# Kernel optimization log

Measured on AMD Instinct MI355X. Metric: run time of the kernel, lower is better.

The kernel has to match this reference:

```python
import jax, jax.numpy as jnp
import numpy as np

N, C, L, D, F = 8, 128, 512, 64, 512
ATTN_W = 64
LN_EPS = 1e-5
ATTN_EPS = 1e-6


def _xavier(k, shape):
    lim = float(np.sqrt(6.0 / (shape[0] + shape[1])))
    return jax.random.uniform(k, shape, jnp.float32, -lim, lim)


def setup_inputs() -> dict:
    key = jax.random.key(0)
    ks = jax.random.split(key, 8)
    return dict(
        x=jax.random.normal(ks[0], (N, C, L), jnp.float32),
        Wx=_xavier(ks[1], (C, D)),
        Wt=_xavier(ks[2], (C, D)),
        bh=jnp.zeros((D,), jnp.float32),
        Wa=_xavier(ks[3], (D, 1)),
        ba=jnp.zeros((1,), jnp.float32),
        W0=_xavier(ks[4], (C, F)),
        b0=jnp.zeros((F,), jnp.float32),
        W1=_xavier(ks[5], (F, C)),
        b1=jnp.zeros((C,), jnp.float32),
        g0=jnp.ones((C,), jnp.float32),
        be0=jnp.zeros((C,), jnp.float32),
        g1=jnp.ones((C,), jnp.float32),
        be1=jnp.zeros((C,), jnp.float32),
    )


def _layernorm(y, g, b):
    mu = jnp.mean(y, axis=-1, keepdims=True)
    var = jnp.var(y, axis=-1, keepdims=True)
    return (y - mu) * jax.lax.rsqrt(var + LN_EPS) * g + b


def reference(x, Wx, Wt, bh, Wa, ba, W0, b0, W1, b1, g0, be0, g1, be1):
    xt = jnp.transpose(x, (0, 2, 1))  # (N, L, C)
    q = jnp.einsum('nlc,cd->nld', xt, Wt)  # (N, L, D)
    k = jnp.einsum('nlc,cd->nld', xt, Wx)  # (N, L, D)
    # additive (Bahdanau) scores: h is the large (N, L, L, D) intermediate
    h = jnp.tanh(q[:, :, None, :] + k[:, None, :, :] + bh)
    e = jnp.einsum('nlmd,d->nlm', h, Wa[:, 0]) + ba[0]  # (N, L, L)
    e = jnp.exp(e - jnp.max(e, axis=-1, keepdims=True))
    # local band mask: tril(w//2 - 1) & triu(-w//2) on (row i, col j)
    dij = jnp.arange(L)[None, :] - jnp.arange(L)[:, None]  # j - i
    mask = (dij <= ATTN_W // 2 - 1) & (dij >= -(ATTN_W // 2))
    e = jnp.where(mask, e, 0.0)
    a = e / (jnp.sum(e, axis=-1, keepdims=True) + ATTN_EPS)  # (N, L, L)
    v = jnp.einsum('nlm,nmc->nlc', a, xt)  # (N, L, C)
    x2 = _layernorm(v + xt, g0, be0)
    x3 = jnp.einsum('nlf,fc->nlc', jax.nn.relu(jnp.einsum('nlc,cf->nlf', x2, W0) + b0), W1) + b1
    x4 = _layernorm(x3 + x2, g1, be1)
    return (jnp.transpose(x4, (0, 2, 1)), a)
```

## Files before the change

### kernel.cpp

```cpp
#include <hip/hip_runtime.h>
#include <cstddef>


__global__ __launch_bounds__(256) void prep_kernel(
    const float* __restrict__ x, const float* __restrict__ Wt,
    const float* __restrict__ Wx, float* __restrict__ xt,
    float* __restrict__ q, float* __restrict__ k) {
  __shared__ float xs[128][17];
  int tid = threadIdx.x;
  int bz = blockIdx.x;
  int n = bz >> 6;
  int t6 = bz & 63;
  int l0 = (t6 >> 1) << 4;
  int which = t6 & 1;

  for (int idx = tid; idx < 512; idx += 256) {
    int c = idx >> 2, v = idx & 3;
    float4 d4 = *(const float4*)(x + ((size_t)n * 128 + c) * 512 + l0 + 4 * v);
    xs[c][4 * v + 0] = d4.x; xs[c][4 * v + 1] = d4.y;
    xs[c][4 * v + 2] = d4.z; xs[c][4 * v + 3] = d4.w;
  }
  __syncthreads();

  if (which == 0) {
    for (int idx = tid; idx < 2048; idx += 256) {
      int c = idx & 127, jj = idx >> 7;
      xt[((size_t)n * 512 + l0 + jj) * 128 + c] = xs[c][jj];
    }
  }

  const float* W = which ? Wx : Wt;
  float* dst = which ? k : q;
  int r = tid >> 4;
  int f0 = (tid & 15) << 2;
  float acc[4] = {0.f, 0.f, 0.f, 0.f};
#pragma unroll 4
  for (int cc = 0; cc < 128; cc++) {
    float xv = xs[cc][r];
    float4 w = *(const float4*)(W + cc * 64 + f0);
    acc[0] += xv * w.x; acc[1] += xv * w.y;
    acc[2] += xv * w.z; acc[3] += xv * w.w;
  }
  *(float4*)(dst + ((size_t)n * 512 + l0 + r) * 64 + f0) =
      make_float4(acc[0], acc[1], acc[2], acc[3]);
}

__global__ __launch_bounds__(512, 4) void attn_ffn_fused_kernel(
    const float* __restrict__ q, const float* __restrict__ k,
    const float* __restrict__ bh, const float* __restrict__ Wa,
    const float* __restrict__ ba, const float* __restrict__ xt,
    const float* __restrict__ g0, const float* __restrict__ be0,
    const float* __restrict__ W0, const float* __restrict__ b0,
    const float* __restrict__ W1, const float* __restrict__ b1,
    const float* __restrict__ g1, const float* __restrict__ be1,
    float* __restrict__ a, float* __restrict__ out) {
  __shared__ __align__(16) char smem[61440];
  __shared__ __align__(16) float xstT[128][12];
  __shared__ __align__(16) float avT[71][10];
  __shared__ __align__(16) float was[64];

  float (*ks)[68] = (float(*)[68])smem;
  float (*qs)[64] = (float(*)[64])(smem + 19328);
  float (*tstT)[12] = (float(*)[12])smem;
  float (*part)[8][128] = (float(*)[8][128])(smem + 24576);
  float (*ys)[128] = (float(*)[128])(smem + 57344);

  int tid = threadIdx.x;
  int w = tid >> 6, lane = tid & 63;
  size_t rbase = (size_t)blockIdx.x * 8;
  int n = (int)(rbase >> 9);
  int i0 = (int)(rbase & 511);
  int jlo0 = i0 - 32;

  if (tid < 64) was[tid] = Wa[tid];
  for (int idx = tid; idx < 71 * 10; idx += 512) ((float*)avT)[idx] = 0.f;
  if (tid < 128) {
    int r = tid >> 4, d4 = (tid & 15) << 2;
    float4 qv = *(const float4*)(q + ((size_t)n * 512 + i0 + r) * 64 + d4);
    float4 bv = *(const float4*)(bh + d4);
    *(float4*)(&qs[r][d4]) =
        make_float4(qv.x + bv.x, qv.y + bv.y, qv.z + bv.z, qv.w + bv.w);
  }
  for (int idx = tid; idx < 71 * 16; idx += 512) {
    int row = idx >> 4, d4 = (idx & 15) << 2;
    int j = jlo0 + row;
    float4 v = make_float4(0.f, 0.f, 0.f, 0.f);
    if (j >= 0 && j < 512)
      v = *(const float4*)(k + ((size_t)n * 512 + j) * 64 + d4);
    *(float4*)(&ks[row][d4]) = v;
  }
  __syncthreads();

  {
    int r = w;
    int i = i0 + r;
    int j = jlo0 + r + lane;
    bool valid = (j >= 0 && j < 512);
    const float* krow = &ks[r + lane][0];
    float e = 0.f;
#pragma unroll
    for (int d4 = 0; d4 < 64; d4 += 4) {
      float4 kv = *(const float4*)(krow + d4);
      float4 qv = *(const float4*)(&qs[r][d4]);
      float4 wv = *(const float4*)(&was[d4]);
      float h0 = qv.x + kv.x, h1 = qv.y + kv.y;
      float h2 = qv.z + kv.z, h3 = qv.w + kv.w;
      float t0 = 1.f - 2.f * __builtin_amdgcn_rcpf(__expf(2.f * h0) + 1.f);
      float t1 = 1.f - 2.f * __builtin_amdgcn_rcpf(__expf(2.f * h1) + 1.f);
      float t2 = 1.f - 2.f * __builtin_amdgcn_rcpf(__expf(2.f * h2) + 1.f);
      float t3 = 1.f - 2.f * __builtin_amdgcn_rcpf(__expf(2.f * h3) + 1.f);
      e += wv.x * t0 + wv.y * t1 + wv.z * t2 + wv.w * t3;
    }
    e += ba[0];
    if (!valid) e = -1e30f;

    float m = e;
    for (int o = 32; o > 0; o >>= 1) m = fmaxf(m, __shfl_xor(m, o, 64));
    float ex = valid ? __expf(e - m) : 0.f;
    float s = ex;
    for (int o = 32; o > 0; o >>= 1) s += __shfl_xor(s, o, 64);
    float aw = ex / (s + 1e-6f);
    avT[r + lane][r] = aw;

    float* arow = a + ((size_t)n * 512 + i) * 512;
    int jlo = i - 32;
#pragma unroll
    for (int t = 0; t < 2; t++) {
      int col0 = 4 * lane + 256 * t;
      float4 v;
      { int jr = col0 + 0 - jlo; int jc = min(max(jr, 0), 63); v.x = (jr >= 0 && jr < 64) ? avT[r + jc][r] : 0.f; }
      { int jr = col0 + 1 - jlo; int jc = min(max(jr, 0), 63); v.y = (jr >= 0 && jr < 64) ? avT[r + jc][r] : 0.f; }
      { int jr = col0 + 2 - jlo; int jc = min(max(jr, 0), 63); v.z = (jr >= 0 && jr < 64) ? avT[r + jc][r] : 0.f; }
      { int jr = col0 + 3 - jlo; int jc = min(max(jr, 0), 63); v.w = (jr >= 0 && jr < 64) ? avT[r + jc][r] : 0.f; }
      *(float4*)(arow + col0) = v;
    }
  }
  __syncthreads();

  {
    int c = tid & 127;
    int rh = tid >> 7;
    int r0 = 2 * rh;
    const float* xtn = xt + (size_t)n * 512 * 128;
    float acc0 = 0.f, acc1 = 0.f;
    for (int col = r0; col <= r0 + 64; col++) {
      int jj = jlo0 + col;
      int jc = min(max(jj, 0), 511);
      float xv = xtn[(size_t)jc * 128 + c];
      float2 av2 = *(const float2*)(&avT[col][r0]);
      acc0 += av2.x * xv;
      acc1 += av2.y * xv;
    }
    float res0 = xtn[(size_t)(i0 + r0) * 128 + c];
    float res1 = xtn[(size_t)(i0 + r0 + 1) * 128 + c];
    *(float2*)(&xstT[c][r0]) = make_float2(acc0 + res0, acc1 + res1);
  }
  __syncthreads();

  {
    float a0 = xstT[lane][w], a1 = xstT[lane + 64][w];
    float s = a0 + a1, s2 = a0 * a0 + a1 * a1;
    for (int o = 32; o > 0; o >>= 1) {
      s += __shfl_xor(s, o, 64);
      s2 += __shfl_xor(s2, o, 64);
    }
    float mu = s * (1.f / 128.f);
    float var = s2 * (1.f / 128.f) - mu * mu;
    float rs = rsqrtf(var + 1e-5f);
    xstT[lane][w] = (a0 - mu) * rs * g0[lane] + be0[lane];
    xstT[lane + 64][w] = (a1 - mu) * rs * g0[lane + 64] + be0[lane + 64];
  }
  __syncthreads();

  {
    int g = lane & 15;
    int kq = lane >> 4;
    int f0 = (16 * w + g) << 2;
    float acc[8][4];
#pragma unroll
    for (int i = 0; i < 8; i++)
#pragma unroll
      for (int u = 0; u < 4; u++) acc[i][u] = 0.f;
    int ccb = kq << 5;
#pragma unroll 4
    for (int cc = ccb; cc < ccb + 32; cc++) {
      float4 xa = *(const float4*)(&xstT[cc][0]);
      float4 xb = *(const float4*)(&xstT[cc][4]);
      float4 wv = *(const float4*)(W0 + (size_t)cc * 512 + f0);
      acc[0][0] += xa.x * wv.x; acc[0][1] += xa.x * wv.y; acc[0][2] += xa.x * wv.z; acc[0][3] += xa.x * wv.w;
      acc[1][0] += xa.y * wv.x; acc[1][1] += xa.y * wv.y; acc[1][2] += xa.y * wv.z; acc[1][3] += xa.y * wv.w;
      acc[2][0] += xa.z * wv.x; acc[2][1] += xa.z * wv.y; acc[2][2] += xa.z * wv.z; acc[2][3] += xa.z * wv.w;
      acc[3][0] += xa.w * wv.x; acc[3][1] += xa.w * wv.y; acc[3][2] += xa.w * wv.z; acc[3][3] += xa.w * wv.w;
      acc[4][0] += xb.x * wv.x; acc[4][1] += xb.x * wv.y; acc[4][2] += xb.x * wv.z; acc[4][3] += xb.x * wv.w;
      acc[5][0] += xb.y * wv.x; acc[5][1] += xb.y * wv.y; acc[5][2] += xb.y * wv.z; acc[5][3] += xb.y * wv.w;
      acc[6][0] += xb.z * wv.x; acc[6][1] += xb.z * wv.y; acc[6][2] += xb.z * wv.z; acc[6][3] += xb.z * wv.w;
      acc[7][0] += xb.w * wv.x; acc[7][1] += xb.w * wv.y; acc[7][2] += xb.w * wv.z; acc[7][3] += xb.w * wv.w;
    }
#pragma unroll
    for (int i = 0; i < 8; i++)
#pragma unroll
      for (int u = 0; u < 4; u++) {
        float v = acc[i][u];
        v += __shfl_xor(v, 16, 64);
        v += __shfl_xor(v, 32, 64);
        acc[i][u] = v;
      }
    int f = f0 + kq;
    float bb = b0[f];
    float r0v[8];
#pragma unroll
    for (int i = 0; i < 8; i++) {
      float v = (kq == 0) ? acc[i][0] : (kq == 1) ? acc[i][1]
              : (kq == 2) ? acc[i][2] : acc[i][3];
      r0v[i] = fmaxf(v + bb, 0.f);
    }
    *(float4*)(&tstT[f][0]) = make_float4(r0v[0], r0v[1], r0v[2], r0v[3]);
    *(float4*)(&tstT[f][4]) = make_float4(r0v[4], r0v[5], r0v[6], r0v[7]);
  }
  __syncthreads();

  {
    int c0 = (lane & 31) << 2;
    int rh = lane >> 5;
    float acc[4][4];
#pragma unroll
    for (int i = 0; i < 4; i++)
#pragma unroll
      for (int u = 0; u < 4; u++) acc[i][u] = 0.f;
    const float* W1p = W1 + (size_t)w * 64 * 128;
    int tb = w << 6;
#pragma unroll 4
    for (int t = 0; t < 64; t++) {
      float4 tv = *(const float4*)(&tstT[tb + t][4 * rh]);
      float4 wv = *(const float4*)(W1p + (size_t)t * 128 + c0);
      acc[0][0] += tv.x * wv.x; acc[0][1] += tv.x * wv.y; acc[0][2] += tv.x * wv.z; acc[0][3] += tv.x * wv.w;
      acc[1][0] += tv.y * wv.x; acc[1][1] += tv.y * wv.y; acc[1][2] += tv.y * wv.z; acc[1][3] += tv.y * wv.w;
      acc[2][0] += tv.z * wv.x; acc[2][1] += tv.z * wv.y; acc[2][2] += tv.z * wv.z; acc[2][3] += tv.z * wv.w;
      acc[3][0] += tv.w * wv.x; acc[3][1] += tv.w * wv.y; acc[3][2] += tv.w * wv.z; acc[3][3] += tv.w * wv.w;
    }
#pragma unroll
    for (int i = 0; i < 4; i++) {
      *(float4*)(&part[w][4 * rh + i][c0]) =
          make_float4(acc[i][0], acc[i][1], acc[i][2], acc[i][3]);
    }
  }
  __syncthreads();

  if (tid < 256) {
    int r = tid >> 5, c0 = (tid & 31) << 2;
    float4 s = make_float4(0.f, 0.f, 0.f, 0.f);
#pragma unroll
    for (int ko = 0; ko < 8; ko++) {
      float4 p = *(const float4*)(&part[ko][r][c0]);
      s.x += p.x; s.y += p.y; s.z += p.z; s.w += p.w;
    }
    float4 bv = *(const float4*)(b1 + c0);
    s.x += bv.x + xstT[c0 + 0][r];
    s.y += bv.y + xstT[c0 + 1][r];
    s.z += bv.z + xstT[c0 + 2][r];
    s.w += bv.w + xstT[c0 + 3][r];
    *(float4*)(&ys[r][c0]) = s;
  }
  __syncthreads();

  {
    float a0 = ys[w][lane], a1 = ys[w][lane + 64];
    float s = a0 + a1, s2 = a0 * a0 + a1 * a1;
    for (int o = 32; o > 0; o >>= 1) {
      s += __shfl_xor(s, o, 64);
      s2 += __shfl_xor(s2, o, 64);
    }
    float mu = s * (1.f / 128.f);
    float var = s2 * (1.f / 128.f) - mu * mu;
    float rs = rsqrtf(var + 1e-5f);
    ys[w][lane] = (a0 - mu) * rs * g1[lane] + be1[lane];
    ys[w][lane + 64] = (a1 - mu) * rs * g1[lane + 64] + be1[lane + 64];
  }
  __syncthreads();

  {
    int c = tid >> 2, tq = tid & 3;
    *(float2*)(out + ((size_t)n * 128 + c) * 512 + i0 + 2 * tq) =
        make_float2(ys[2 * tq][c], ys[2 * tq + 1][c]);
  }
}

extern "C" void kernel_launch(void* const* d_in, const int* in_sizes, int n_in,
                              void* d_out, int out_size, void* d_ws, size_t ws_size,
                              hipStream_t stream) {
  const float* x   = (const float*)d_in[0];
  const float* Wx  = (const float*)d_in[1];
  const float* Wt  = (const float*)d_in[2];
  const float* bh  = (const float*)d_in[3];
  const float* Wa  = (const float*)d_in[4];
  const float* ba  = (const float*)d_in[5];
  const float* W0  = (const float*)d_in[6];
  const float* b0  = (const float*)d_in[7];
  const float* W1  = (const float*)d_in[8];
  const float* b1  = (const float*)d_in[9];
  const float* g0  = (const float*)d_in[10];
  const float* be0 = (const float*)d_in[11];
  const float* g1  = (const float*)d_in[12];
  const float* be1 = (const float*)d_in[13];

  float* outx = (float*)d_out;
  float* outa = outx + (size_t)524288;

  float* ws = (float*)d_ws;
  float* xt = ws;
  float* q  = xt + 524288;
  float* k  = q + 262144;

  prep_kernel<<<512, 256, 0, stream>>>(x, Wt, Wx, xt, q, k);
  attn_ffn_fused_kernel<<<512, 512, 0, stream>>>(
      q, k, bh, Wa, ba, xt, g0, be0, W0, b0, W1, b1, g1, be1, outa, outx);
}
```

Baseline: 124.9 us.

## Drop xt workspace, stage x window in shared memory and prefetch FFN weights

The prep kernel no longer writes a transposed copy of x to global memory. Instead each attention block loads its 72-row window of x directly into a padded shared tile and uses it for the banded weighted sum and the residual. The prep kernel now computes q and k together in one 512-thread block. The W0/W1 loops gain register double-buffered weight prefetch, and the bias plus residual reduction is fused into the second layernorm, which removes one barrier. The cost is more shared memory packed into overlapping smem regions, and strided uncoalesced global reads when filling the x tile.

Result: no change. 124.7 us (-0.1%).

```diff
diff --git a/kernel.cpp b/kernel.cpp
--- a/kernel.cpp
+++ b/kernel.cpp
@@ -2,37 +2,29 @@
 #include <cstddef>
 
 
-__global__ __launch_bounds__(256) void prep_kernel(
+__global__ __launch_bounds__(512) void prep_kernel(
     const float* __restrict__ x, const float* __restrict__ Wt,
-    const float* __restrict__ Wx, float* __restrict__ xt,
-    float* __restrict__ q, float* __restrict__ k) {
+    const float* __restrict__ Wx, float* __restrict__ q,
+    float* __restrict__ k) {
   __shared__ float xs[128][17];
   int tid = threadIdx.x;
-  int bz = blockIdx.x;
-  int n = bz >> 6;
-  int t6 = bz & 63;
-  int l0 = (t6 >> 1) << 4;
-  int which = t6 & 1;
-
-  for (int idx = tid; idx < 512; idx += 256) {
-    int c = idx >> 2, v = idx & 3;
+  int n = blockIdx.x >> 5;
+  int l0 = (blockIdx.x & 31) << 4;
+
+  {
+    int c = tid >> 2, v = tid & 3;
     float4 d4 = *(const float4*)(x + ((size_t)n * 128 + c) * 512 + l0 + 4 * v);
     xs[c][4 * v + 0] = d4.x; xs[c][4 * v + 1] = d4.y;
     xs[c][4 * v + 2] = d4.z; xs[c][4 * v + 3] = d4.w;
   }
   __syncthreads();
 
-  if (which == 0) {
-    for (int idx = tid; idx < 2048; idx += 256) {
-      int c = idx & 127, jj = idx >> 7;
-      xt[((size_t)n * 512 + l0 + jj) * 128 + c] = xs[c][jj];
-    }
-  }
-
-  const float* W = which ? Wx : Wt;
-  float* dst = which ? k : q;
-  int r = tid >> 4;
-  int f0 = (tid & 15) << 2;
+  int half = tid >> 8;
+  int t = tid & 255;
+  int r = t >> 4;
+  int f0 = (t & 15) << 2;
+  const float* W = half ? Wx : Wt;
+  float* dst = half ? k : q;
   float acc[4] = {0.f, 0.f, 0.f, 0.f};
 #pragma unroll 4
   for (int cc = 0; cc < 128; cc++) {
@@ -46,9 +38,9 @@
 }
 
 __global__ __launch_bounds__(512, 4) void attn_ffn_fused_kernel(
-    const float* __restrict__ q, const float* __restrict__ k,
-    const float* __restrict__ bh, const float* __restrict__ Wa,
-    const float* __restrict__ ba, const float* __restrict__ xt,
+    const float* __restrict__ x, const float* __restrict__ q,
+    const float* __restrict__ k, const float* __restrict__ bh,
+    const float* __restrict__ Wa, const float* __restrict__ ba,
     const float* __restrict__ g0, const float* __restrict__ be0,
     const float* __restrict__ W0, const float* __restrict__ b0,
     const float* __restrict__ W1, const float* __restrict__ b1,
@@ -60,7 +52,8 @@
   __shared__ __align__(16) float was[64];
 
   float (*ks)[68] = (float(*)[68])smem;
-  float (*qs)[64] = (float(*)[64])(smem + 19328);
+  float (*qs)[64] = (float(*)[64])(smem + 19312);
+  float (*xtw)[132] = (float(*)[132])(smem + 21360);
   float (*tstT)[12] = (float(*)[12])smem;
   float (*part)[8][128] = (float(*)[8][128])(smem + 24576);
   float (*ys)[128] = (float(*)[128])(smem + 57344);
@@ -88,6 +81,24 @@
     if (j >= 0 && j < 512)
       v = *(const float4*)(k + ((size_t)n * 512 + j) * 64 + d4);
     *(float4*)(&ks[row][d4]) = v;
+  }
+  for (int t = tid; t < 128 * 18; t += 512) {
+    int c = t / 18;
+    int u = t - c * 18;
+    int row = 4 * u;
+    int j0 = jlo0 + row;
+    const float* xp = x + ((size_t)n * 128 + c) * 512;
+    float4 v = make_float4(0.f, 0.f, 0.f, 0.f);
+    if (j0 >= 0 && j0 + 3 < 512) {
+      v = *(const float4*)(xp + j0);
+    } else {
+      if (j0 + 0 >= 0 && j0 + 0 < 512) v.x = xp[j0 + 0];
+      if (j0 + 1 >= 0 && j0 + 1 < 512) v.y = xp[j0 + 1];
+      if (j0 + 2 >= 0 && j0 + 2 < 512) v.z = xp[j0 + 2];
+      if (j0 + 3 >= 0 && j0 + 3 < 512) v.w = xp[j0 + 3];
+    }
+    xtw[row + 0][c] = v.x; xtw[row + 1][c] = v.y;
+    xtw[row + 2][c] = v.z; xtw[row + 3][c] = v.w;
   }
   __syncthreads();
 
@@ -119,8 +130,7 @@
     float ex = valid ? __expf(e - m) : 0.f;
     float s = ex;
     for (int o = 32; o > 0; o >>= 1) s += __shfl_xor(s, o, 64);
-    float aw = ex / (s + 1e-6f);
-    avT[r + lane][r] = aw;
+    avT[r + lane][r] = ex / (s + 1e-6f);
 
     float* arow = a + ((size_t)n * 512 + i) * 512;
     int jlo = i - 32;
@@ -139,20 +149,18 @@
 
   {
     int c = tid & 127;
-    int rh = tid >> 7;
-    int r0 = 2 * rh;
-    const float* xtn = xt + (size_t)n * 512 * 128;
+    int r0 = (tid >> 7) << 1;
     float acc0 = 0.f, acc1 = 0.f;
-    for (int col = r0; col <= r0 + 64; col++) {
-      int jj = jlo0 + col;
-      int jc = min(max(jj, 0), 511);
-      float xv = xtn[(size_t)jc * 128 + c];
+#pragma unroll 5
+    for (int m = 0; m < 65; m++) {
+      int col = r0 + m;
+      float xv = xtw[col][c];
       float2 av2 = *(const float2*)(&avT[col][r0]);
       acc0 += av2.x * xv;
       acc1 += av2.y * xv;
     }
-    float res0 = xtn[(size_t)(i0 + r0) * 128 + c];
-    float res1 = xtn[(size_t)(i0 + r0 + 1) * 128 + c];
+    float res0 = xtw[32 + r0][c];
+    float res1 = xtw[33 + r0][c];
     *(float2*)(&xstT[c][r0]) = make_float2(acc0 + res0, acc1 + res1);
   }
   __syncthreads();
@@ -176,25 +184,41 @@
     int g = lane & 15;
     int kq = lane >> 4;
     int f0 = (16 * w + g) << 2;
+    int ccb = kq << 5;
+    const float* w0p = W0 + (size_t)ccb * 512 + f0;
     float acc[8][4];
 #pragma unroll
     for (int i = 0; i < 8; i++)
 #pragma unroll
       for (int u = 0; u < 4; u++) acc[i][u] = 0.f;
-    int ccb = kq << 5;
-#pragma unroll 4
-    for (int cc = ccb; cc < ccb + 32; cc++) {
-      float4 xa = *(const float4*)(&xstT[cc][0]);
-      float4 xb = *(const float4*)(&xstT[cc][4]);
-      float4 wv = *(const float4*)(W0 + (size_t)cc * 512 + f0);
-      acc[0][0] += xa.x * wv.x; acc[0][1] += xa.x * wv.y; acc[0][2] += xa.x * wv.z; acc[0][3] += xa.x * wv.w;
-      acc[1][0] += xa.y * wv.x; acc[1][1] += xa.y * wv.y; acc[1][2] += xa.y * wv.z; acc[1][3] += xa.y * wv.w;
-      acc[2][0] += xa.z * wv.x; acc[2][1] += xa.z * wv.y; acc[2][2] += xa.z * wv.z; acc[2][3] += xa.z * wv.w;
-      acc[3][0] += xa.w * wv.x; acc[3][1] += xa.w * wv.y; acc[3][2] += xa.w * wv.z; acc[3][3] += xa.w * wv.w;
-      acc[4][0] += xb.x * wv.x; acc[4][1] += xb.x * wv.y; acc[4][2] += xb.x * wv.z; acc[4][3] += xb.x * wv.w;
-      acc[5][0] += xb.y * wv.x; acc[5][1] += xb.y * wv.y; acc[5][2] += xb.y * wv.z; acc[5][3] += xb.y * wv.w;
-      acc[6][0] += xb.z * wv.x; acc[6][1] += xb.z * wv.y; acc[6][2] += xb.z * wv.z; acc[6][3] += xb.z * wv.w;
-      acc[7][0] += xb.w * wv.x; acc[7][1] += xb.w * wv.y; acc[7][2] += xb.w * wv.z; acc[7][3] += xb.w * wv.w;
+
+    float4 wbuf[4];
+#pragma unroll
+    for (int p = 0; p < 4; p++)
+      wbuf[p] = *(const float4*)(w0p + (size_t)p * 512);
+#pragma unroll
+    for (int c4 = 0; c4 < 8; c4++) {
+      float4 cur0 = wbuf[0], cur1 = wbuf[1], cur2 = wbuf[2], cur3 = wbuf[3];
+      if (c4 < 7) {
+#pragma unroll
+        for (int p = 0; p < 4; p++)
+          wbuf[p] = *(const float4*)(w0p + (size_t)((c4 + 1) * 4 + p) * 512);
+      }
+#pragma unroll
+      for (int p = 0; p < 4; p++) {
+        int cc = ccb + c4 * 4 + p;
+        float4 wv = (p == 0) ? cur0 : (p == 1) ? cur1 : (p == 2) ? cur2 : cur3;
+        float4 xa = *(const float4*)(&xstT[cc][0]);
+        float4 xb = *(const float4*)(&xstT[cc][4]);
+        acc[0][0] += xa.x * wv.x; acc[0][1] += xa.x * wv.y; acc[0][2] += xa.x * wv.z; acc[0][3] += xa.x * wv.w;
+        acc[1][0] += xa.y * wv.x; acc[1][1] += xa.y * wv.y; acc[1][2] += xa.y * wv.z; acc[1][3] += xa.y * wv.w;
+        acc[2][0] += xa.z * wv.x; acc[2][1] += xa.z * wv.y; acc[2][2] += xa.z * wv.z; acc[2][3] += xa.z * wv.w;
+        acc[3][0] += xa.w * wv.x; acc[3][1] += xa.w * wv.y; acc[3][2] += xa.w * wv.z; acc[3][3] += xa.w * wv.w;
+        acc[4][0] += xb.x * wv.x; acc[4][1] += xb.x * wv.y; acc[4][2] += xb.x * wv.z; acc[4][3] += xb.x * wv.w;
+        acc[5][0] += xb.y * wv.x; acc[5][1] += xb.y * wv.y; acc[5][2] += xb.y * wv.z; acc[5][3] += xb.y * wv.w;
+        acc[6][0] += xb.z * wv.x; acc[6][1] += xb.z * wv.y; acc[6][2] += xb.z * wv.z; acc[6][3] += xb.z * wv.w;
+        acc[7][0] += xb.w * wv.x; acc[7][1] += xb.w * wv.y; acc[7][2] += xb.w * wv.z; acc[7][3] += xb.w * wv.w;
+      }
     }
 #pragma unroll
     for (int i = 0; i < 8; i++)
@@ -222,21 +246,36 @@
   {
     int c0 = (lane & 31) << 2;
     int rh = lane >> 5;
+    const float* W1p = W1 + (size_t)w * 64 * 128 + c0;
+    int tb = w << 6;
     float acc[4][4];
 #pragma unroll
     for (int i = 0; i < 4; i++)
 #pragma unroll
       for (int u = 0; u < 4; u++) acc[i][u] = 0.f;
-    const float* W1p = W1 + (size_t)w * 64 * 128;
-    int tb = w << 6;
-#pragma unroll 4
-    for (int t = 0; t < 64; t++) {
-      float4 tv = *(const float4*)(&tstT[tb + t][4 * rh]);
-      float4 wv = *(const float4*)(W1p + (size_t)t * 128 + c0);
-      acc[0][0] += tv.x * wv.x; acc[0][1] += tv.x * wv.y; acc[0][2] += tv.x * wv.z; acc[0][3] += tv.x * wv.w;
-      acc[1][0] += tv.y * wv.x; acc[1][1] += tv.y * wv.y; acc[1][2] += tv.y * wv.z; acc[1][3] += tv.y * wv.w;
-      acc[2][0] += tv.z * wv.x; acc[2][1] += tv.z * wv.y; acc[2][2] += tv.z * wv.z; acc[2][3] += tv.z * wv.w;
-      acc[3][0] += tv.w * wv.x; acc[3][1] += tv.w * wv.y; acc[3][2] += tv.w * wv.z; acc[3][3] += tv.w * wv.w;
+
+    float4 wbuf[4];
+#pragma unroll
+    for (int p = 0; p < 4; p++)
+      wbuf[p] = *(const float4*)(W1p + (size_t)p * 128);
+#pragma unroll
+    for (int t4 = 0; t4 < 16; t4++) {
+      float4 cur0 = wbuf[0], cur1 = wbuf[1], cur2 = wbuf[2], cur3 = wbuf[3];
+      if (t4 < 15) {
+#pragma unroll
+        for (int p = 0; p < 4; p++)
+          wbuf[p] = *(const float4*)(W1p + (size_t)((t4 + 1) * 4 + p) * 128);
+      }
+#pragma unroll
+      for (int p = 0; p < 4; p++) {
+        int t = t4 * 4 + p;
+        float4 wv = (p == 0) ? cur0 : (p == 1) ? cur1 : (p == 2) ? cur2 : cur3;
+        float4 tv = *(const float4*)(&tstT[tb + t][4 * rh]);
+        acc[0][0] += tv.x * wv.x; acc[0][1] += tv.x * wv.y; acc[0][2] += tv.x * wv.z; acc[0][3] += tv.x * wv.w;
+        acc[1][0] += tv.y * wv.x; acc[1][1] += tv.y * wv.y; acc[1][2] += tv.y * wv.z; acc[1][3] += tv.y * wv.w;
+        acc[2][0] += tv.z * wv.x; acc[2][1] += tv.z * wv.y; acc[2][2] += tv.z * wv.z; acc[2][3] += tv.z * wv.w;
+        acc[3][0] += tv.w * wv.x; acc[3][1] += tv.w * wv.y; acc[3][2] += tv.w * wv.z; acc[3][3] += tv.w * wv.w;
+      }
     }
 #pragma unroll
     for (int i = 0; i < 4; i++) {
@@ -246,25 +285,14 @@
   }
   __syncthreads();
 
-  if (tid < 256) {
-    int r = tid >> 5, c0 = (tid & 31) << 2;
-    float4 s = make_float4(0.f, 0.f, 0.f, 0.f);
+  {
+    float a0 = b1[lane] + xstT[lane][w];
+    float a1 = b1[lane + 64] + xstT[lane + 64][w];
 #pragma unroll
     for (int ko = 0; ko < 8; ko++) {
-      float4 p = *(const float4*)(&part[ko][r][c0]);
-      s.x += p.x; s.y += p.y; s.z += p.z; s.w += p.w;
-    }
-    float4 bv = *(const float4*)(b1 + c0);
-    s.x += bv.x + xstT[c0 + 0][r];
-    s.y += bv.y + xstT[c0 + 1][r];
-    s.z += bv.z + xstT[c0 + 2][r];
-    s.w += bv.w + xstT[c0 + 3][r];
-    *(float4*)(&ys[r][c0]) = s;
-  }
-  __syncthreads();
-
-  {
-    float a0 = ys[w][lane], a1 = ys[w][lane + 64];
+      a0 += part[ko][w][lane];
+      a1 += part[ko][w][lane + 64];
+    }
     float s = a0 + a1, s2 = a0 * a0 + a1 * a1;
     for (int o = 32; o > 0; o >>= 1) {
       s += __shfl_xor(s, o, 64);
@@ -307,11 +335,10 @@
   float* outa = outx + (size_t)524288;
 
   float* ws = (float*)d_ws;
-  float* xt = ws;
-  float* q  = xt + 524288;
+  float* q  = ws;
   float* k  = q + 262144;
 
-  prep_kernel<<<512, 256, 0, stream>>>(x, Wt, Wx, xt, q, k);
+  prep_kernel<<<256, 512, 0, stream>>>(x, Wt, Wx, q, k);
   attn_ffn_fused_kernel<<<512, 512, 0, stream>>>(
-      q, k, bh, Wa, ba, xt, g0, be0, W0, b0, W1, b1, g1, be1, outa, outx);
+      x, q, k, bh, Wa, ba, g0, be0, W0, b0, W1, b1, g1, be1, outa, outx);
 }
```
